# Kernel tuning notes

Hardware: AMD Instinct MI355X
Metric: run time of the kernel (lower is better)

## Reference

```python
import jax, jax.numpy as jnp
import numpy as np

BITS = 4
PACK = 32 // BITS  # 8 nibbles per int32
MASK = (1 << BITS) - 1


def _dequant_gptq(qweight, qzeros, scales):
    """GPTQ int4 dequantization matching MixedPrecisionLinear._dequantize_gptq_weight.

    qweight: [OC//PACK, IC] int32 (nibbles packed along output-channel rows)
    qzeros:  [G, IC//PACK]  int32 (nibbles packed along IC columns)
    scales:  [G, IC]        float32
    returns: [OC, IC]       float32 dequantized weight (pre-transpose)
    """
    Rp, IC = qweight.shape
    OC = Rp * PACK
    G = qzeros.shape[0]
    g = OC // G  # group size along OC

    # Unpack weights: row r*PACK + k comes from packed row r, shift k*BITS
    shifts = jnp.arange(PACK, dtype=jnp.int32) * BITS  # [PACK]
    Wq = ((qweight[:, None, :] >> shifts[None, :, None]) & MASK).reshape(OC, IC)

    # Unpack zero points per (group, ic)
    col = jnp.arange(IC, dtype=jnp.int32)
    qz_cols = qzeros[:, col // PACK]                       # [G, IC]
    zp = (qz_cols >> ((col % PACK) * BITS)[None, :]) & MASK  # [G, IC]

    zp_full = jnp.repeat(zp, g, axis=0)                    # [OC, IC]
    scales_full = jnp.repeat(scales, g, axis=0)            # [OC, IC]
    return (Wq - zp_full).astype(jnp.float32) * scales_full


def setup_inputs() -> dict:
    key = jax.random.key(0)
    k0, k1, k2, k3, k4 = jax.random.split(key, 5)
    IN, OUT, G = 4096, 11008, 32   # in_features (OC, packed), out_features (IC), groups
    N = 4096                        # flattened batch*seq tokens
    qweight = jax.random.randint(k0, (IN // PACK, OUT), 0, 2147483647, dtype=jnp.int32)
    qzeros = jax.random.randint(k1, (G, OUT // PACK), 0, 2147483647, dtype=jnp.int32)
    scales = jax.random.uniform(k2, (G, OUT), dtype=jnp.float32) * 0.01
    x = jax.random.normal(k3, (N, IN), dtype=jnp.float32)
    bias = jax.random.normal(k4, (OUT,), dtype=jnp.float32) * 0.01
    return {"input": x, "qweight": qweight, "qzeros": qzeros, "scales": scales, "bias": bias}


def reference(input, qweight, qzeros, scales, bias):
    # W_deq is [OC=in_features, IC=out_features]; the module returns W_deq.t() as the
    # linear weight, so F.linear(input, W_deq.t()) == input @ W_deq + bias.
    W = _dequant_gptq(qweight, qzeros, scales)
    return input @ W + bias
```

## Files before the change

### kernel.cpp

```cpp
#include <hip/hip_runtime.h>
#include <hip/hip_bf16.h>
#include <stdint.h>

#define M_DIM 4096
#define N_DIM 11008
#define K_DIM 4096

typedef float f32x4 __attribute__((ext_vector_type(4)));
typedef __bf16 bf16x8 __attribute__((ext_vector_type(8)));
typedef unsigned short u16x8 __attribute__((ext_vector_type(8)));
typedef unsigned short u16x4 __attribute__((ext_vector_type(4)));

typedef __attribute__((address_space(1))) const unsigned int guint;
typedef __attribute__((address_space(3))) unsigned int luint;
#define GLOAD_LDS16(g, l) \
    __builtin_amdgcn_global_load_lds((guint*)(g), (luint*)(l), 16, 0, 0)

#define WAIT_VM4() asm volatile("s_waitcnt vmcnt(4)" ::: "memory")
#define WAIT_VM2() asm volatile("s_waitcnt vmcnt(2)" ::: "memory")
#define WAIT_VM0() asm volatile("s_waitcnt vmcnt(0)" ::: "memory")

__device__ __forceinline__ unsigned short f2bf(float f) {
    union { float f; unsigned u; } v; v.f = f;
    return (unsigned short)((v.u + 0x7FFFu + ((v.u >> 16) & 1u)) >> 16);
}

__global__ void __launch_bounds__(256) cvt_x_kernel(
    const float* __restrict__ X, __hip_bfloat16* __restrict__ Y)
{
    const size_t i = ((size_t)blockIdx.x * 256 + threadIdx.x) * 8;
    f32x4 a = *reinterpret_cast<const f32x4*>(X + i);
    f32x4 b = *reinterpret_cast<const f32x4*>(X + i + 4);
    bf16x8 h;
    #pragma unroll
    for (int e = 0; e < 4; ++e) { h[e] = (__bf16)a[e]; h[e + 4] = (__bf16)b[e]; }
    *reinterpret_cast<bf16x8*>(Y + i) = h;
}

__global__ void __launch_bounds__(256) dequant_kernel(
    const int* __restrict__ QW, const int* __restrict__ QZ,
    const float* __restrict__ SC, __hip_bfloat16* __restrict__ Wt)
{
    const int n   = blockIdx.x * 64 + (threadIdx.x & 63);
    const int k64 = blockIdx.y * 4 + (threadIdx.x >> 6);
    const int g   = k64 >> 1;
    const int zp  = ((unsigned)QZ[g * (N_DIM / 8) + (n >> 3)] >> ((n & 7) << 2)) & 15;
    const float sc = SC[g * N_DIM + n];
    const float zs = (float)zp * sc;
    #pragma unroll
    for (int r = 0; r < 8; ++r) {
        const unsigned qw = (unsigned)QW[(size_t)(k64 * 8 + r) * N_DIM + n];
        bf16x8 h;
        #pragma unroll
        for (int j = 0; j < 8; ++j)
            h[j] = (__bf16)((float)((qw >> (j * 4)) & 15u) * sc - zs);
        *reinterpret_cast<bf16x8*>(Wt + (size_t)n * K_DIM + k64 * 64 + r * 8) = h;
    }
}

__global__ void __launch_bounds__(1024, 4) gemm_bf16_kernel(
    const __hip_bfloat16* __restrict__ A,
    const __hip_bfloat16* __restrict__ Bt,
    const float* __restrict__ BIAS, float* __restrict__ OUT)
{
    extern __shared__ unsigned char lds[];

    const int tid  = threadIdx.x;
    const int wave = tid >> 6;
    const int lane = tid & 63;
    const int l15  = lane & 15;
    const int lhi  = lane >> 4;
    const int wr   = wave >> 2;
    const int wc   = wave & 3;

    const int bid = blockIdx.x;
    const int swz = (bid & 7) * 86 + (bid >> 3);
    const int m0  = (swz & 15) * 256;
    const int n0  = (swz >> 4) * 256;

    const int r_loc = wave * 16 + (lane >> 2);
    const int kswz8 = ((lane & 3) ^ ((lane >> 3) & 3)) * 8;
    const __hip_bfloat16* Asrc = A  + (size_t)(m0 + r_loc) * K_DIM + kswz8;
    const __hip_bfloat16* Bsrc = Bt + (size_t)(n0 + r_loc) * K_DIM + kswz8;
    const int ldst = wave * 1024;

    const int slotx = ((lhi ^ ((l15 >> 1) & 3)) << 4);
    int aoff[4], boff[4];
    #pragma unroll
    for (int i = 0; i < 4; ++i)
        aoff[i] = (wr * 64 + i * 16 + l15) * 64 + slotx;
    #pragma unroll
    for (int j = 0; j < 4; ++j)
        boff[j] = 16384 + (wc * 64 + j * 16 + l15) * 64 + slotx;

    f32x4 acc[4][4] = {};

    auto stage = [&](int c) {
        const int buf = (c & 3) * 32768;
        const size_t kof = (size_t)c * 32;
        GLOAD_LDS16(Asrc + kof, lds + buf + ldst);
        GLOAD_LDS16(Bsrc + kof, lds + buf + 16384 + ldst);
    };

    auto compute = [&](int buf) {
        bf16x8 afr[4], bfr[4];
        #pragma unroll
        for (int j = 0; j < 4; ++j)
            bfr[j] = *reinterpret_cast<const bf16x8*>(lds + buf + boff[j]);
        #pragma unroll
        for (int i = 0; i < 4; ++i)
            afr[i] = *reinterpret_cast<const bf16x8*>(lds + buf + aoff[i]);
        __builtin_amdgcn_s_setprio(1);
        #pragma unroll
        for (int i = 0; i < 4; ++i)
            #pragma unroll
            for (int j = 0; j < 4; ++j)
                acc[i][j] = __builtin_amdgcn_mfma_f32_16x16x32_bf16(
                    afr[i], bfr[j], acc[i][j], 0, 0, 0);
        __builtin_amdgcn_s_setprio(0);
    };

    stage(0); stage(1); stage(2);

    for (int c = 0; c < 125; ++c) {
        WAIT_VM4();
        __builtin_amdgcn_s_barrier();
        __builtin_amdgcn_sched_barrier(0);
        stage(c + 3);
        compute((c & 3) * 32768);
    }
    WAIT_VM4();
    __builtin_amdgcn_s_barrier();
    __builtin_amdgcn_sched_barrier(0);
    compute((125 & 3) * 32768);
    WAIT_VM2();
    __builtin_amdgcn_s_barrier();
    __builtin_amdgcn_sched_barrier(0);
    compute((126 & 3) * 32768);
    WAIT_VM0();
    __builtin_amdgcn_s_barrier();
    __builtin_amdgcn_sched_barrier(0);
    compute((127 & 3) * 32768);

    #pragma unroll
    for (int j = 0; j < 4; ++j) {
        const int n    = n0 + wc * 64 + j * 16 + l15;
        const float bv = BIAS[n];
        #pragma unroll
        for (int i = 0; i < 4; ++i) {
            const int mb = m0 + wr * 64 + i * 16 + (lhi << 2);
            #pragma unroll
            for (int t = 0; t < 4; ++t)
                OUT[(size_t)(mb + t) * N_DIM + n] = acc[i][j][t] + bv;
        }
    }
}

__global__ void __launch_bounds__(256) gptq_gemm_kernel(
    const float* __restrict__ X, const int* __restrict__ QW,
    const int* __restrict__ QZ, const float* __restrict__ SC,
    const float* __restrict__ BIAS, float* __restrict__ OUT)
{
    __shared__ __align__(16) unsigned char slds[32768];
    const int tid  = threadIdx.x;
    const int n0   = blockIdx.x * 128;
    const int m0   = blockIdx.y * 128;
    const int wave = tid >> 6;
    const int lane = tid & 63;
    const int wm   = (wave >> 1) * 64;
    const int wn   = (wave & 1) * 64;
    const int l15  = lane & 15;
    const int lhi  = lane >> 4;
    const int arow  = tid >> 4;
    const int acol4 = (tid & 15) << 2;
    const int bnl   = tid & 127;
    const int brb   = tid >> 7;
    const int col   = n0 + bnl;

    f32x4 acc[4][4] = {};
    for (int kt = 0; kt < K_DIM / 64; ++kt) {
        const int k0 = kt * 64;
        #pragma unroll
        for (int r8 = 0; r8 < 8; ++r8) {
            const int row = (r8 << 4) + arow;
            f32x4 v = *reinterpret_cast<const f32x4*>(
                X + (size_t)(m0 + row) * K_DIM + (k0 + acol4));
            u16x4 h;
            #pragma unroll
            for (int e = 0; e < 4; ++e) h[e] = f2bf(v[e]);
            const int bo = row * 128 + ((acol4 << 1) ^ ((row & 7) << 4));
            *reinterpret_cast<u16x4*>(slds + bo) = h;
        }
        {
            const int g    = k0 >> 7;
            const int zp   = (((unsigned)QZ[g * (N_DIM / 8) + (col >> 3)])
                              >> ((col & 7) << 2)) & 15;
            const float sc = SC[g * N_DIM + col];
            const float zs = (float)zp * sc;
            #pragma unroll
            for (int rb = 0; rb < 4; ++rb) {
                const int rl = (rb << 1) + brb;
                const unsigned qw =
                    (unsigned)QW[(size_t)((k0 >> 3) + rl) * N_DIM + col];
                u16x8 h;
                #pragma unroll
                for (int j = 0; j < 8; ++j) {
                    float w = (float)((qw >> (j << 2)) & 15u) * sc - zs;
                    h[j] = f2bf(w);
                }
                const int bo = 16384 + bnl * 128 + ((rl << 4) ^ ((bnl & 7) << 4));
                *reinterpret_cast<u16x8*>(slds + bo) = h;
            }
        }
        __syncthreads();
        #pragma unroll
        for (int kk = 0; kk < 2; ++kk) {
            bf16x8 afr[4], bfr[4];
            #pragma unroll
            for (int i = 0; i < 4; ++i) {
                const int row = wm + (i << 4) + l15;
                afr[i] = *reinterpret_cast<const bf16x8*>(
                    slds + row * 128 + (((kk << 6) + (lhi << 4)) ^ ((row & 7) << 4)));
            }
            #pragma unroll
            for (int j = 0; j < 4; ++j) {
                const int n = wn + (j << 4) + l15;
                bfr[j] = *reinterpret_cast<const bf16x8*>(
                    slds + 16384 + n * 128 + (((kk << 6) + (lhi << 4)) ^ ((n & 7) << 4)));
            }
            #pragma unroll
            for (int i = 0; i < 4; ++i)
                #pragma unroll
                for (int j = 0; j < 4; ++j)
                    acc[i][j] = __builtin_amdgcn_mfma_f32_16x16x32_bf16(
                        afr[i], bfr[j], acc[i][j], 0, 0, 0);
        }
        __syncthreads();
    }
    #pragma unroll
    for (int j = 0; j < 4; ++j) {
        const int n    = n0 + wn + (j << 4) + l15;
        const float bv = BIAS[n];
        #pragma unroll
        for (int i = 0; i < 4; ++i) {
            const int mb = m0 + wm + (i << 4) + (lhi << 2);
            #pragma unroll
            for (int t = 0; t < 4; ++t)
                OUT[(size_t)(mb + t) * N_DIM + n] = acc[i][j][t] + bv;
        }
    }
}

extern "C" void kernel_launch(void* const* d_in, const int* in_sizes, int n_in,
                              void* d_out, int out_size, void* d_ws, size_t ws_size,
                              hipStream_t stream) {
    const float* X  = (const float*)d_in[0];
    const int*   QW = (const int*)d_in[1];
    const int*   QZ = (const int*)d_in[2];
    const float* SC = (const float*)d_in[3];
    const float* BI = (const float*)d_in[4];
    float*      OUT = (float*)d_out;

    const size_t xbf_bytes = (size_t)M_DIM * K_DIM * 2;
    const size_t wt_bytes  = (size_t)N_DIM * K_DIM * 2;

    if (ws_size >= xbf_bytes + wt_bytes) {
        __hip_bfloat16* Xbf = (__hip_bfloat16*)d_ws;
        __hip_bfloat16* Wt  = (__hip_bfloat16*)((char*)d_ws + xbf_bytes);

        cvt_x_kernel<<<(M_DIM * K_DIM) / (256 * 8), 256, 0, stream>>>(X, Xbf);
        dequant_kernel<<<dim3(N_DIM / 64, K_DIM / 256), 256, 0, stream>>>(QW, QZ, SC, Wt);
        gemm_bf16_kernel<<<dim3((M_DIM / 256) * (N_DIM / 256)), 1024, 131072, stream>>>(
            Xbf, Wt, BI, OUT);
    } else {
        gptq_gemm_kernel<<<dim3(N_DIM / 128, M_DIM / 128), 256, 0, stream>>>(
            X, QW, QZ, SC, BI, OUT);
    }
}
```

Baseline: 406.3 us.

## Merge prep kernels and switch GEMM to persistent atomic work-stealing tiles

Fuses the activation conversion and weight dequantization into one launch, and batches the eight qweight loads per thread before converting them. The GEMM becomes a persistent 512-block kernel that takes 128x256 tiles from an atomic counter. The old 256x256 tiles with a 4-stage LDS ring are replaced by 512-thread blocks with double-buffered static LDS. This is meant to cut launch overhead and tail imbalance, but the smaller tiles and shallower pipeline may lower operand reuse and hide less latency.

```diff
diff --git a/kernel.cpp b/kernel.cpp
--- a/kernel.cpp
+++ b/kernel.cpp
@@ -16,8 +16,7 @@
 #define GLOAD_LDS16(g, l) \
     __builtin_amdgcn_global_load_lds((guint*)(g), (luint*)(l), 16, 0, 0)
 
-#define WAIT_VM4() asm volatile("s_waitcnt vmcnt(4)" ::: "memory")
-#define WAIT_VM2() asm volatile("s_waitcnt vmcnt(2)" ::: "memory")
+#define WAIT_VM3() asm volatile("s_waitcnt vmcnt(3)" ::: "memory")
 #define WAIT_VM0() asm volatile("s_waitcnt vmcnt(0)" ::: "memory")
 
 __device__ __forceinline__ unsigned short f2bf(float f) {
@@ -25,45 +24,66 @@
     return (unsigned short)((v.u + 0x7FFFu + ((v.u >> 16) & 1u)) >> 16);
 }
 
-__global__ void __launch_bounds__(256) cvt_x_kernel(
-    const float* __restrict__ X, __hip_bfloat16* __restrict__ Y)
+#define DQ_BLOCKS  ((N_DIM / 64) * (K_DIM / 256))
+#define CVT_BLOCKS 2048
+#define CVT_TOTAL  ((size_t)M_DIM * K_DIM)
+
+__global__ void __launch_bounds__(256) prep_kernel(
+    const float* __restrict__ X, const int* __restrict__ QW,
+    const int* __restrict__ QZ, const float* __restrict__ SC,
+    __hip_bfloat16* __restrict__ Xbf, __hip_bfloat16* __restrict__ Wt,
+    int* __restrict__ counter)
 {
-    const size_t i = ((size_t)blockIdx.x * 256 + threadIdx.x) * 8;
-    f32x4 a = *reinterpret_cast<const f32x4*>(X + i);
-    f32x4 b = *reinterpret_cast<const f32x4*>(X + i + 4);
-    bf16x8 h;
-    #pragma unroll
-    for (int e = 0; e < 4; ++e) { h[e] = (__bf16)a[e]; h[e + 4] = (__bf16)b[e]; }
-    *reinterpret_cast<bf16x8*>(Y + i) = h;
-}
-
-__global__ void __launch_bounds__(256) dequant_kernel(
-    const int* __restrict__ QW, const int* __restrict__ QZ,
-    const float* __restrict__ SC, __hip_bfloat16* __restrict__ Wt)
-{
-    const int n   = blockIdx.x * 64 + (threadIdx.x & 63);
-    const int k64 = blockIdx.y * 4 + (threadIdx.x >> 6);
-    const int g   = k64 >> 1;
-    const int zp  = ((unsigned)QZ[g * (N_DIM / 8) + (n >> 3)] >> ((n & 7) << 2)) & 15;
-    const float sc = SC[g * N_DIM + n];
-    const float zs = (float)zp * sc;
-    #pragma unroll
-    for (int r = 0; r < 8; ++r) {
-        const unsigned qw = (unsigned)QW[(size_t)(k64 * 8 + r) * N_DIM + n];
-        bf16x8 h;
-        #pragma unroll
-        for (int j = 0; j < 8; ++j)
-            h[j] = (__bf16)((float)((qw >> (j * 4)) & 15u) * sc - zs);
-        *reinterpret_cast<bf16x8*>(Wt + (size_t)n * K_DIM + k64 * 64 + r * 8) = h;
-    }
-}
-
-__global__ void __launch_bounds__(1024, 4) gemm_bf16_kernel(
+    const int bid = blockIdx.x;
+    if (bid == 0 && threadIdx.x == 0) *counter = 0;
+    if (bid >= CVT_BLOCKS) {
+        const int db  = bid - CVT_BLOCKS;
+        const int bx  = db % (N_DIM / 64);
+        const int by  = db / (N_DIM / 64);
+        const int n   = bx * 64 + (threadIdx.x & 63);
+        const int k64 = by * 4 + (threadIdx.x >> 6);
+        const int g   = k64 >> 1;
+        const int zp  = ((unsigned)QZ[g * (N_DIM / 8) + (n >> 3)]
+                         >> ((n & 7) << 2)) & 15;
+        const float sc = SC[g * N_DIM + n];
+        const float zs = (float)zp * sc;
+        unsigned qv[8];
+        #pragma unroll
+        for (int r = 0; r < 8; ++r)
+            qv[r] = (unsigned)QW[(size_t)(k64 * 8 + r) * N_DIM + n];
+        #pragma unroll
+        for (int r = 0; r < 8; ++r) {
+            bf16x8 h;
+            #pragma unroll
+            for (int j = 0; j < 8; ++j)
+                h[j] = (__bf16)((float)((qv[r] >> (j * 4)) & 15u) * sc - zs);
+            *reinterpret_cast<bf16x8*>(Wt + (size_t)n * K_DIM + k64 * 64 + r * 8) = h;
+        }
+    } else {
+        const size_t nthreads = (size_t)CVT_BLOCKS * 256;
+        size_t i = ((size_t)bid * 256 + threadIdx.x) * 8;
+        const size_t stride = nthreads * 8;
+        for (; i < CVT_TOTAL; i += stride) {
+            f32x4 a = *reinterpret_cast<const f32x4*>(X + i);
+            f32x4 b = *reinterpret_cast<const f32x4*>(X + i + 4);
+            bf16x8 h;
+            #pragma unroll
+            for (int e = 0; e < 4; ++e) { h[e] = (__bf16)a[e]; h[e + 4] = (__bf16)b[e]; }
+            *reinterpret_cast<bf16x8*>(Xbf + i) = h;
+        }
+    }
+}
+
+#define NTILES ((M_DIM / 128) * (N_DIM / 256))
+
+__global__ void __launch_bounds__(512, 4) gemm_ws_kernel(
     const __hip_bfloat16* __restrict__ A,
     const __hip_bfloat16* __restrict__ Bt,
-    const float* __restrict__ BIAS, float* __restrict__ OUT)
+    const float* __restrict__ BIAS, float* __restrict__ OUT,
+    int* __restrict__ counter)
 {
-    extern __shared__ unsigned char lds[];
+    __shared__ __align__(16) unsigned char lds[49152];
+    __shared__ int s_tile;
 
     const int tid  = threadIdx.x;
     const int wave = tid >> 6;
@@ -73,86 +93,87 @@
     const int wr   = wave >> 2;
     const int wc   = wave & 3;
 
-    const int bid = blockIdx.x;
-    const int swz = (bid & 7) * 86 + (bid >> 3);
-    const int m0  = (swz & 15) * 256;
-    const int n0  = (swz >> 4) * 256;
-
-    const int r_loc = wave * 16 + (lane >> 2);
-    const int kswz8 = ((lane & 3) ^ ((lane >> 3) & 3)) * 8;
-    const __hip_bfloat16* Asrc = A  + (size_t)(m0 + r_loc) * K_DIM + kswz8;
-    const __hip_bfloat16* Bsrc = Bt + (size_t)(n0 + r_loc) * K_DIM + kswz8;
-    const int ldst = wave * 1024;
-
-    const int slotx = ((lhi ^ ((l15 >> 1) & 3)) << 4);
+    const int arow = tid >> 2;
+    const int kof  = ((tid & 3) ^ ((tid >> 3) & 3)) * 8;
+    const int t16  = tid * 16;
+
+    const int sws = (lhi ^ ((l15 >> 1) & 3)) << 4;
     int aoff[4], boff[4];
     #pragma unroll
     for (int i = 0; i < 4; ++i)
-        aoff[i] = (wr * 64 + i * 16 + l15) * 64 + slotx;
+        aoff[i] = (wr * 64 + i * 16 + l15) * 64 + sws;
     #pragma unroll
     for (int j = 0; j < 4; ++j)
-        boff[j] = 16384 + (wc * 64 + j * 16 + l15) * 64 + slotx;
-
-    f32x4 acc[4][4] = {};
-
-    auto stage = [&](int c) {
-        const int buf = (c & 3) * 32768;
-        const size_t kof = (size_t)c * 32;
-        GLOAD_LDS16(Asrc + kof, lds + buf + ldst);
-        GLOAD_LDS16(Bsrc + kof, lds + buf + 16384 + ldst);
-    };
-
-    auto compute = [&](int buf) {
-        bf16x8 afr[4], bfr[4];
-        #pragma unroll
-        for (int j = 0; j < 4; ++j)
-            bfr[j] = *reinterpret_cast<const bf16x8*>(lds + buf + boff[j]);
-        #pragma unroll
-        for (int i = 0; i < 4; ++i)
-            afr[i] = *reinterpret_cast<const bf16x8*>(lds + buf + aoff[i]);
-        __builtin_amdgcn_s_setprio(1);
-        #pragma unroll
-        for (int i = 0; i < 4; ++i)
+        boff[j] = 8192 + (wc * 64 + j * 16 + l15) * 64 + sws;
+
+    for (;;) {
+        if (tid == 0) s_tile = atomicAdd(counter, 1);
+        __syncthreads();
+        const int t = s_tile;
+        if (t >= NTILES) break;
+        const int m0 = (t & 31) * 128;
+        const int n0 = (t >> 5) * 256;
+
+        const __hip_bfloat16* Asrc = A  + (size_t)(m0 + arow) * K_DIM + kof;
+        const __hip_bfloat16* Bsrc = Bt + (size_t)(n0 + arow) * K_DIM + kof;
+
+        f32x4 acc[4][4] = {};
+
+        auto stage = [&](int c) {
+            const int buf = (c & 1) * 24576;
+            const size_t k = (size_t)c * 32;
+            GLOAD_LDS16(Asrc + k,                        lds + buf + t16);
+            GLOAD_LDS16(Bsrc + k,                        lds + buf + 8192 + t16);
+            GLOAD_LDS16(Bsrc + k + (size_t)128 * K_DIM,  lds + buf + 8192 + 8192 + t16);
+        };
+        auto compute = [&](int buf) {
+            bf16x8 afr[4], bfr[4];
             #pragma unroll
             for (int j = 0; j < 4; ++j)
-                acc[i][j] = __builtin_amdgcn_mfma_f32_16x16x32_bf16(
-                    afr[i], bfr[j], acc[i][j], 0, 0, 0);
-        __builtin_amdgcn_s_setprio(0);
-    };
-
-    stage(0); stage(1); stage(2);
-
-    for (int c = 0; c < 125; ++c) {
-        WAIT_VM4();
+                bfr[j] = *reinterpret_cast<const bf16x8*>(lds + buf + boff[j]);
+            #pragma unroll
+            for (int i = 0; i < 4; ++i)
+                afr[i] = *reinterpret_cast<const bf16x8*>(lds + buf + aoff[i]);
+            __builtin_amdgcn_s_setprio(1);
+            #pragma unroll
+            for (int i = 0; i < 4; ++i)
+                #pragma unroll
+                for (int j = 0; j < 4; ++j)
+                    acc[i][j] = __builtin_amdgcn_mfma_f32_16x16x32_bf16(
+                        afr[i], bfr[j], acc[i][j], 0, 0, 0);
+            __builtin_amdgcn_s_setprio(0);
+        };
+
+        stage(0); stage(1);
+
+        for (int c = 0; c < 126; ++c) {
+            WAIT_VM3();
+            __builtin_amdgcn_s_barrier();
+            compute((c & 1) * 24576);
+            __builtin_amdgcn_s_barrier();
+            stage(c + 2);
+        }
+        WAIT_VM3();
         __builtin_amdgcn_s_barrier();
-        __builtin_amdgcn_sched_barrier(0);
-        stage(c + 3);
-        compute((c & 3) * 32768);
-    }
-    WAIT_VM4();
-    __builtin_amdgcn_s_barrier();
-    __builtin_amdgcn_sched_barrier(0);
-    compute((125 & 3) * 32768);
-    WAIT_VM2();
-    __builtin_amdgcn_s_barrier();
-    __builtin_amdgcn_sched_barrier(0);
-    compute((126 & 3) * 32768);
-    WAIT_VM0();
-    __builtin_amdgcn_s_barrier();
-    __builtin_amdgcn_sched_barrier(0);
-    compute((127 & 3) * 32768);
-
-    #pragma unroll
-    for (int j = 0; j < 4; ++j) {
-        const int n    = n0 + wc * 64 + j * 16 + l15;
-        const float bv = BIAS[n];
-        #pragma unroll
-        for (int i = 0; i < 4; ++i) {
-            const int mb = m0 + wr * 64 + i * 16 + (lhi << 2);
-            #pragma unroll
-            for (int t = 0; t < 4; ++t)
-                OUT[(size_t)(mb + t) * N_DIM + n] = acc[i][j][t] + bv;
-        }
+        compute(0);
+        __builtin_amdgcn_s_barrier();
+        WAIT_VM0();
+        __builtin_amdgcn_s_barrier();
+        compute(24576);
+
+        #pragma unroll
+        for (int j = 0; j < 4; ++j) {
+            const int n    = n0 + wc * 64 + j * 16 + l15;
+            const float bv = BIAS[n];
+            #pragma unroll
+            for (int i = 0; i < 4; ++i) {
+                const int mb = m0 + wr * 64 + i * 16 + (lhi << 2);
+                #pragma unroll
+                for (int e = 0; e < 4; ++e)
+                    OUT[(size_t)(mb + e) * N_DIM + n] = acc[i][j][e] + bv;
+            }
+        }
+        __syncthreads();
     }
 }
 
@@ -263,15 +284,16 @@
 
     const size_t xbf_bytes = (size_t)M_DIM * K_DIM * 2;
     const size_t wt_bytes  = (size_t)N_DIM * K_DIM * 2;
-
-    if (ws_size >= xbf_bytes + wt_bytes) {
+    const size_t cnt_off   = xbf_bytes + wt_bytes;
+
+    if (ws_size >= cnt_off + 16) {
         __hip_bfloat16* Xbf = (__hip_bfloat16*)d_ws;
         __hip_bfloat16* Wt  = (__hip_bfloat16*)((char*)d_ws + xbf_bytes);
-
-        cvt_x_kernel<<<(M_DIM * K_DIM) / (256 * 8), 256, 0, stream>>>(X, Xbf);
-        dequant_kernel<<<dim3(N_DIM / 64, K_DIM / 256), 256, 0, stream>>>(QW, QZ, SC, Wt);
-        gemm_bf16_kernel<<<dim3((M_DIM / 256) * (N_DIM / 256)), 1024, 131072, stream>>>(
-            Xbf, Wt, BI, OUT);
+        int*            cnt = (int*)((char*)d_ws + cnt_off);
+
+        prep_kernel<<<DQ_BLOCKS + CVT_BLOCKS, 256, 0, stream>>>(
+            X, QW, QZ, SC, Xbf, Wt, cnt);
+        gemm_ws_kernel<<<512, 512, 0, stream>>>(Xbf, Wt, BI, OUT, cnt);
     } else {
         gptq_gemm_kernel<<<dim3(N_DIM / 128, M_DIM / 128), 256, 0, stream>>>(
             X, QW, QZ, SC, BI, OUT);
```

After: 458.7 us. 1.13x slower.
